# Performance work log

Hardware: AMD Instinct MI355X
Metric: run time of the kernel (lower is better)

Reference implementation:

```python
import jax, jax.numpy as jnp
import numpy as np

FMAP = 160        # feature-map side -> N = FMAP*FMAP anchors
STRIDE = 4.0      # anchor grid stride in pixels
ANCHOR_SIZE = 32.0
NUM_CLASSES = 8
MAX_GT = 50
BATCH = 32


def setup_inputs() -> dict:
    key = jax.random.key(0)
    k0, k1, k2, k3, k4, k5 = jax.random.split(key, 6)
    B, C, H = BATCH, NUM_CLASSES, FMAP
    cls_output = jax.random.normal(k0, (B, C, 1, H, H), jnp.float32)
    reg_output = jax.random.normal(k1, (B, 4, 1, H, H), jnp.float32) * 0.3
    # anchor grid: one ANCHOR_SIZE box per feature-map cell; flatten order
    # matches torch's reshape over (H, W)
    c = (jnp.arange(H, dtype=jnp.float32) + 0.5) * STRIDE
    cy, cx = jnp.meshgrid(c, c, indexing='ij')   # row-major [H, W]
    cx = cx.reshape(-1); cy = cy.reshape(-1)
    half = ANCHOR_SIZE / 2.0
    anchors = jnp.stack([cx - half, cy - half, cx + half, cy + half], axis=1)
    # padded GT boxes, all geometrically valid (x1<x2, y1<y2)
    cxy = jax.random.uniform(k2, (B, MAX_GT, 2), jnp.float32, 64.0, 576.0)
    wh = jax.random.uniform(k3, (B, MAX_GT, 2), jnp.float32, 16.0, 128.0)
    gt_boxes = jnp.concatenate([cxy - wh / 2.0, cxy + wh / 2.0], axis=-1)
    gt_labels = jax.random.randint(k4, (B, MAX_GT), 0, NUM_CLASSES)
    num_boxes = jax.random.randint(k5, (B,), 0, MAX_GT + 1)
    return dict(cls_output=cls_output, reg_output=reg_output, anchors=anchors,
                gt_boxes=gt_boxes, gt_labels=gt_labels, num_boxes=num_boxes)


def _decode_boxes(reg, anchors):
    # inverse of the encoding in the loss: tx=(gt_cx-a_cx)*(4/aw) then (tx+1)/2
    aw = anchors[:, 2] - anchors[:, 0]
    ah = anchors[:, 3] - anchors[:, 1]
    acx = anchors[:, 0] + 0.5 * aw
    acy = anchors[:, 1] + 0.5 * ah
    tx = reg[..., 0] * 2.0 - 1.0
    ty = reg[..., 1] * 2.0 - 1.0
    cx = acx + tx * aw / 4.0
    cy = acy + ty * ah / 4.0
    w = aw * jnp.exp(reg[..., 2])
    h = ah * jnp.exp(reg[..., 3])
    return jnp.stack([cx - w / 2, cy - h / 2, cx + w / 2, cy + h / 2], axis=-1)


def _pairwise_iou(b1, b2):
    # b1 [B,N,4], b2 [B,M,4] -> [B,N,M]
    lt = jnp.maximum(b1[:, :, None, :2], b2[:, None, :, :2])
    rb = jnp.minimum(b1[:, :, None, 2:], b2[:, None, :, 2:])
    wh = jnp.clip(rb - lt, 0.0)
    inter = wh[..., 0] * wh[..., 1]
    a1 = (b1[..., 2] - b1[..., 0]) * (b1[..., 3] - b1[..., 1])
    a2 = (b2[..., 2] - b2[..., 0]) * (b2[..., 3] - b2[..., 1])
    return inter / jnp.maximum(a1[:, :, None] + a2[:, None, :] - inter, 1e-8)


def _smooth_l1(x):
    ax = jnp.abs(x)
    return jnp.where(ax < 1.0, 0.5 * x * x, ax - 0.5)


def _forward(cls_output, reg_output, anchors, gt_boxes, gt_labels, num_boxes):
    B, C = cls_output.shape[0], cls_output.shape[1]
    M = gt_boxes.shape[1]
    cls_i = cls_output.reshape(B, C, -1).transpose(0, 2, 1)   # [B,N,C]
    reg_i = reg_output.reshape(B, 4, -1).transpose(0, 2, 1)   # [B,N,4]
    decoded = _decode_boxes(reg_i, anchors)                    # [B,N,4]
    ious = _pairwise_iou(decoded, gt_boxes)                    # [B,N,M]
    valid = jnp.arange(M)[None, :] < num_boxes[:, None]        # [B,M]
    ious = jnp.where(valid[:, None, :], ious, -1.0)
    max_ious = ious.max(axis=-1)                               # [B,N]
    max_idx = ious.argmax(axis=-1)                             # [B,N]
    has = num_boxes > 0                                        # [B]
    pos = (max_ious >= 0.25) & has[:, None]
    neg = (max_ious < 0.1) & has[:, None]
    # classification
    logp = jax.nn.log_softmax(cls_i, axis=-1)
    tgt = jnp.take_along_axis(gt_labels, max_idx, axis=1)      # [B,N]
    ce_tgt = -jnp.take_along_axis(logp, tgt[..., None], axis=-1)[..., 0]
    ce_bg = -logp[..., 0]
    posf = pos.astype(cls_i.dtype)
    negf = neg.astype(cls_i.dtype)
    npos = posf.sum(-1)
    nneg = negf.sum(-1)
    cls_pos = jnp.where(npos > 0, (ce_tgt * posf).sum(-1) / jnp.maximum(npos, 1.0), 0.0)
    cls_neg = jnp.where(nneg > 0, (ce_bg * negf).sum(-1) / jnp.maximum(nneg, 1.0), 0.0)
    cls_losses = jnp.where(has, cls_pos + cls_neg, ce_bg.mean(-1))
    pg = jnp.take_along_axis(gt_boxes, max_idx[..., None], axis=1)  # [B,N,4]
    aw = anchors[:, 2] - anchors[:, 0]
    ah = anchors[:, 3] - anchors[:, 1]
    acx = anchors[:, 0] + 0.5 * aw
    acy = anchors[:, 1] + 0.5 * ah
    gw = pg[..., 2] - pg[..., 0]
    gh = pg[..., 3] - pg[..., 1]
    gcx = pg[..., 0] + 0.5 * gw
    gcy = pg[..., 1] + 0.5 * gh
    tx = ((gcx - acx) * (4.0 / aw) + 1.0) / 2.0
    ty = ((gcy - acy) * (4.0 / ah) + 1.0) / 2.0
    tw = jnp.log(jnp.maximum(gw, 1e-6) / aw)
    th = jnp.log(jnp.maximum(gh, 1e-6) / ah)
    reg_t = jnp.stack([tx, ty, tw, th], axis=-1)               # [B,N,4]
    sl = _smooth_l1(reg_i - reg_t)
    reg_losses = jnp.where(npos > 0,
                           (sl * posf[..., None]).sum((-1, -2)) / jnp.maximum(npos * 4.0, 1.0),
                           0.0)
    total_pos = npos.sum()
    cls_final = cls_losses.mean()
    reg_final = reg_losses.sum() / jnp.maximum(total_pos, 1.0)
    return cls_final + reg_final, cls_final, reg_final, total_pos


def reference(cls_output, reg_output, anchors, gt_boxes, gt_labels, num_boxes):
    return _forward(cls_output, reg_output, anchors, gt_boxes, gt_labels, num_boxes)
```

## Files before the change

kernel.cpp:

```cpp
#include <hip/hip_runtime.h>

#define FMAP 160
#define NANCH (FMAP * FMAP)
#define NCLS 8
#define MAXGT 50
#define BATCH 32
#define NT 256
#define TILES 5
#define BLOCKS_PER_B (TILES * TILES)
#define PSTRIDE 8

__device__ __forceinline__ float fc(const float4& v, int k) {
    return k == 0 ? v.x : k == 1 ? v.y : k == 2 ? v.z : v.w;
}
__device__ __forceinline__ float sl1(float x) {
    float ax = fabsf(x);
    return ax < 1.f ? 0.5f * x * x : ax - 0.5f;
}

__global__ __launch_bounds__(NT) void detloss_main(
    const float* __restrict__ cls, const float* __restrict__ reg,
    const float* __restrict__ gtb, const int* __restrict__ gtl,
    const int* __restrict__ nb, float* __restrict__ partials)
{
    const int b  = blockIdx.y;
    const int t  = threadIdx.x;
    const int bx = blockIdx.x;
    const int tx = bx % TILES, ty = bx / TILES;
    const int w  = t >> 6, l = t & 63;
    const int R  = ty * 32 + w * 8 + (l >> 3);
    const int G  = tx * 8 + (l & 7);
    const int vt = R * (FMAP / 4) + G;

    const float4* regv = (const float4*)(reg + (size_t)b * 4 * NANCH);
    float4 rx = regv[0 * (NANCH / 4) + vt];
    float4 ry = regv[1 * (NANCH / 4) + vt];
    float4 rw = regv[2 * (NANCH / 4) + vt];
    float4 rh = regv[3 * (NANCH / 4) + vt];
    const float4* clsv = (const float4*)(cls + (size_t)b * NCLS * NANCH);
    float4 L[NCLS];
#pragma unroll
    for (int c = 0; c < NCLS; c++) L[c] = clsv[c * (NANCH / 4) + vt];

    __shared__ float4 gbox[64];
    __shared__ float  garea[64];
    __shared__ int    glab[64];
    if (t < MAXGT) {
        float4 g = ((const float4*)gtb)[b * MAXGT + t];
        gbox[t]  = g;
        garea[t] = (g.z - g.x) * (g.w - g.y);
        glab[t]  = gtl[b * MAXGT + t];
    }
    const int num = nb[b];

    const float acx0 = (float)((G * 4) * 4 + 2);
    const float acy  = (float)(R * 4 + 2);

    float x0[4], y0[4], x1[4], y1[4], a1[4];
#pragma unroll
    for (int k = 0; k < 4; k++) {
        float acx = acx0 + 4.f * (float)k;
        float txr = fc(rx, k) * 2.f - 1.f;
        float tyr = fc(ry, k) * 2.f - 1.f;
        float cx = acx + txr * 8.f;
        float cy = acy + tyr * 8.f;
        float ww = 32.f * __expf(fc(rw, k));
        float hh = 32.f * __expf(fc(rh, k));
        x0[k] = cx - 0.5f * ww; y0[k] = cy - 0.5f * hh;
        x1[k] = cx + 0.5f * ww; y1[k] = cy + 0.5f * hh;
        a1[k] = ww * hh;
    }

    float lse[4], cebg[4];
#pragma unroll
    for (int k = 0; k < 4; k++) {
        float s = 0.f;
#pragma unroll
        for (int c = 0; c < NCLS; c++) s += __expf(fc(L[c], k));
        lse[k]  = __logf(s);
        cebg[k] = lse[k] - fc(L[0], k);
    }

    float bx0 = fminf(fminf(x0[0], x0[1]), fminf(x0[2], x0[3]));
    float by0 = fminf(fminf(y0[0], y0[1]), fminf(y0[2], y0[3]));
    float bx1 = fmaxf(fmaxf(x1[0], x1[1]), fmaxf(x1[2], x1[3]));
    float by1 = fmaxf(fmaxf(y1[0], y1[1]), fmaxf(y1[2], y1[3]));
#pragma unroll
    for (int o = 1; o < 64; o <<= 1) {
        bx0 = fminf(bx0, __shfl_xor(bx0, o, 64));
        by0 = fminf(by0, __shfl_xor(by0, o, 64));
        bx1 = fmaxf(bx1, __shfl_xor(bx1, o, 64));
        by1 = fmaxf(by1, __shfl_xor(by1, o, 64));
    }

    __syncthreads();

    float4 gme = gbox[l];
    bool pass = (l < num) && (gme.x <= bx1) && (gme.z >= bx0)
                          && (gme.y <= by1) && (gme.w >= by0);
    unsigned long long mask = __ballot(pass);

    float bi[4] = {-1.f, -1.f, -1.f, -1.f};
    float bu[4] = { 1.f,  1.f,  1.f,  1.f};
    int   bidx[4] = {0, 0, 0, 0};
    while (mask) {
        int m = (int)__builtin_ctzll(mask);
        mask &= mask - 1;
        float4 g  = gbox[m];
        float  ga = garea[m];
#pragma unroll
        for (int k = 0; k < 4; k++) {
            float ltx = fmaxf(x0[k], g.x), lty = fmaxf(y0[k], g.y);
            float rbx = fminf(x1[k], g.z), rby = fminf(y1[k], g.w);
            float wx = fmaxf(rbx - ltx, 0.f), wy = fmaxf(rby - lty, 0.f);
            float inter = wx * wy;
            float u = a1[k] + ga - inter;
            bool better = inter * bu[k] > bi[k] * u;
            bi[k]   = better ? inter : bi[k];
            bu[k]   = better ? u     : bu[k];
            bidx[k] = better ? m     : bidx[k];
        }
    }

    float s_pk = 0.f, s_cp = 0.f, s_cn = 0.f, s_bg = 0.f, s_sl = 0.f;
    const bool has = num > 0;
#pragma unroll
    for (int k = 0; k < 4; k++) {
        s_bg += cebg[k];
        bool pos = has && (bi[k] >= 0.25f * bu[k]);
        bool neg = has && (bi[k] < 0.1f * bu[k]);
        s_pk += pos ? 1.f : (neg ? 4096.f : 0.f);
        s_cn += neg ? cebg[k] : 0.f;
        if (pos) {
            int tg = glab[bidx[k]];
            float e0 = (tg & 1) ? fc(L[1], k) : fc(L[0], k);
            float e1 = (tg & 1) ? fc(L[3], k) : fc(L[2], k);
            float e2 = (tg & 1) ? fc(L[5], k) : fc(L[4], k);
            float e3 = (tg & 1) ? fc(L[7], k) : fc(L[6], k);
            float f0 = (tg & 2) ? e1 : e0;
            float f1 = (tg & 2) ? e3 : e2;
            float ltg = (tg & 4) ? f1 : f0;
            s_cp += lse[k] - ltg;
            float4 gp = gbox[bidx[k]];
            float gw = gp.z - gp.x, gh = gp.w - gp.y;
            float gcx = gp.x + 0.5f * gw, gcy = gp.y + 0.5f * gh;
            float acx = acx0 + 4.f * (float)k;
            float txt = ((gcx - acx) * 0.125f + 1.f) * 0.5f;
            float tyt = ((gcy - acy) * 0.125f + 1.f) * 0.5f;
            float twt = __logf(fmaxf(gw, 1e-6f) * 0.03125f);
            float tht = __logf(fmaxf(gh, 1e-6f) * 0.03125f);
            s_sl += sl1(fc(rx, k) - txt) + sl1(fc(ry, k) - tyt)
                  + sl1(fc(rw, k) - twt) + sl1(fc(rh, k) - tht);
        }
    }

#pragma unroll
    for (int o = 32; o > 0; o >>= 1) {
        s_pk += __shfl_down(s_pk, o, 64);
        s_cp += __shfl_down(s_cp, o, 64);
        s_cn += __shfl_down(s_cn, o, 64);
        s_bg += __shfl_down(s_bg, o, 64);
        s_sl += __shfl_down(s_sl, o, 64);
    }
    __shared__ float red[4][5];
    if (l == 0) {
        red[w][0] = s_pk; red[w][1] = s_cp; red[w][2] = s_cn;
        red[w][3] = s_bg; red[w][4] = s_sl;
    }
    __syncthreads();
    if (t == 0) {
        float* p = partials + (size_t)(b * BLOCKS_PER_B + bx) * PSTRIDE;
        float4 v = make_float4(red[0][0] + red[1][0] + red[2][0] + red[3][0],
                               red[0][1] + red[1][1] + red[2][1] + red[3][1],
                               red[0][2] + red[1][2] + red[2][2] + red[3][2],
                               red[0][3] + red[1][3] + red[2][3] + red[3][3]);
        *(float4*)p = v;
        p[4] = red[0][4] + red[1][4] + red[2][4] + red[3][4];
    }
}

__global__ __launch_bounds__(256) void detloss_final(
    const float* __restrict__ partials, const int* __restrict__ nb,
    float* __restrict__ out)
{
    const int t = threadIdx.x;
    const int img = t >> 3, sub = t & 7;
    float np = 0.f, nn = 0.f, cp = 0.f, cn = 0.f, bg = 0.f, sl = 0.f;
#pragma unroll
    for (int j = 0; j < 4; ++j) {
        int blk = sub + (j << 3);
        if (blk < BLOCKS_PER_B) {
            const float* p = partials + (size_t)(img * BLOCKS_PER_B + blk) * PSTRIDE;
            float pk  = p[0];
            float nnv = floorf(pk * (1.f / 4096.f));
            np += pk - 4096.f * nnv;
            nn += nnv;
            cp += p[1]; cn += p[2]; bg += p[3]; sl += p[4];
        }
    }
#pragma unroll
    for (int o = 4; o > 0; o >>= 1) {
        np += __shfl_down(np, o, 8);
        nn += __shfl_down(nn, o, 8);
        cp += __shfl_down(cp, o, 8);
        cn += __shfl_down(cn, o, 8);
        bg += __shfl_down(bg, o, 8);
        sl += __shfl_down(sl, o, 8);
    }
    __shared__ float acc[32][4];
    if (sub == 0) {
        bool hasb = nb[img] > 0;
        float clsb;
        if (hasb) {
            float a = (np > 0.f) ? cp / fmaxf(np, 1.f) : 0.f;
            float c = (nn > 0.f) ? cn / fmaxf(nn, 1.f) : 0.f;
            clsb = a + c;
        } else {
            clsb = bg / (float)NANCH;
        }
        float regb = (np > 0.f) ? sl / fmaxf(np * 4.f, 1.f) : 0.f;
        acc[img][0] = clsb; acc[img][1] = regb; acc[img][2] = np;
    }
    __syncthreads();
    if (t < 64) {
        float c = 0.f, r = 0.f, tp = 0.f;
        if (t < 32) { c = acc[t][0]; r = acc[t][1]; tp = acc[t][2]; }
#pragma unroll
        for (int o = 32; o > 0; o >>= 1) {
            c  += __shfl_down(c,  o, 64);
            r  += __shfl_down(r,  o, 64);
            tp += __shfl_down(tp, o, 64);
        }
        if (t == 0) {
            float clsf = c / (float)BATCH;
            float regf = r / fmaxf(tp, 1.f);
            out[0] = clsf + regf;
            out[1] = clsf;
            out[2] = regf;
            out[3] = tp;
        }
    }
}

extern "C" void kernel_launch(void* const* d_in, const int* in_sizes, int n_in,
                              void* d_out, int out_size, void* d_ws, size_t ws_size,
                              hipStream_t stream) {
    const float* cls = (const float*)d_in[0];
    const float* reg = (const float*)d_in[1];
    const float* gtb = (const float*)d_in[3];
    const int*   gtl = (const int*)d_in[4];
    const int*   nb  = (const int*)d_in[5];
    float* out      = (float*)d_out;
    float* partials = (float*)d_ws;

    dim3 grid(BLOCKS_PER_B, BATCH);
    detloss_main<<<grid, NT, 0, stream>>>(cls, reg, gtb, gtl, nb, partials);
    detloss_final<<<1, 256, 0, stream>>>(partials, nb, out);
}
```

Before: 19.53 us.

## Fuse main and final kernels via cooperative launch with grid sync

Moves the per-tile work and the final reduction into device functions and runs them in one cooperative kernel separated by a grid-wide barrier, so the second kernel launch goes away. A fallback to the two-kernel path stays in place for when occupancy cannot hold all 800 blocks at once. Each call now adds host-side occupancy and attribute queries, and the cooperative launch plus grid sync carry their own overhead.

```diff
diff --git a/kernel.cpp b/kernel.cpp
--- a/kernel.cpp
+++ b/kernel.cpp
@@ -1,4 +1,7 @@
 #include <hip/hip_runtime.h>
+#include <hip/hip_cooperative_groups.h>
+
+namespace cg = cooperative_groups;
 
 #define FMAP 160
 #define NANCH (FMAP * FMAP)
@@ -18,14 +21,12 @@
     return ax < 1.f ? 0.5f * x * x : ax - 0.5f;
 }
 
-__global__ __launch_bounds__(NT) void detloss_main(
+__device__ __forceinline__ void tile_work(
     const float* __restrict__ cls, const float* __restrict__ reg,
     const float* __restrict__ gtb, const int* __restrict__ gtl,
-    const int* __restrict__ nb, float* __restrict__ partials)
-{
-    const int b  = blockIdx.y;
-    const int t  = threadIdx.x;
-    const int bx = blockIdx.x;
+    const int* __restrict__ nb, float* __restrict__ partials,
+    int b, int bx, int t)
+{
     const int tx = bx % TILES, ty = bx / TILES;
     const int w  = t >> 6, l = t & 63;
     const int R  = ty * 32 + w * 8 + (l >> 3);
@@ -176,14 +177,14 @@
                                red[0][3] + red[1][3] + red[2][3] + red[3][3]);
         *(float4*)p = v;
         p[4] = red[0][4] + red[1][4] + red[2][4] + red[3][4];
-    }
-}
-
-__global__ __launch_bounds__(256) void detloss_final(
+        __threadfence();
+    }
+}
+
+__device__ __forceinline__ void finalize_work(
     const float* __restrict__ partials, const int* __restrict__ nb,
-    float* __restrict__ out)
-{
-    const int t = threadIdx.x;
+    float* __restrict__ out, int t)
+{
     const int img = t >> 3, sub = t & 7;
     float np = 0.f, nn = 0.f, cp = 0.f, cn = 0.f, bg = 0.f, sl = 0.f;
 #pragma unroll
@@ -242,6 +243,33 @@
     }
 }
 
+__global__ __launch_bounds__(NT, 4) void detloss_coop(
+    const float* __restrict__ cls, const float* __restrict__ reg,
+    const float* __restrict__ gtb, const int* __restrict__ gtl,
+    const int* __restrict__ nb, float* __restrict__ partials,
+    float* __restrict__ out)
+{
+    tile_work(cls, reg, gtb, gtl, nb, partials, blockIdx.y, blockIdx.x, threadIdx.x);
+    cg::this_grid().sync();
+    if (blockIdx.x == 0 && blockIdx.y == 0)
+        finalize_work(partials, nb, out, threadIdx.x);
+}
+
+__global__ __launch_bounds__(NT) void detloss_main(
+    const float* __restrict__ cls, const float* __restrict__ reg,
+    const float* __restrict__ gtb, const int* __restrict__ gtl,
+    const int* __restrict__ nb, float* __restrict__ partials)
+{
+    tile_work(cls, reg, gtb, gtl, nb, partials, blockIdx.y, blockIdx.x, threadIdx.x);
+}
+
+__global__ __launch_bounds__(NT) void detloss_final(
+    const float* __restrict__ partials, const int* __restrict__ nb,
+    float* __restrict__ out)
+{
+    finalize_work(partials, nb, out, threadIdx.x);
+}
+
 extern "C" void kernel_launch(void* const* d_in, const int* in_sizes, int n_in,
                               void* d_out, int out_size, void* d_ws, size_t ws_size,
                               hipStream_t stream) {
@@ -254,6 +282,20 @@
     float* partials = (float*)d_ws;
 
     dim3 grid(BLOCKS_PER_B, BATCH);
-    detloss_main<<<grid, NT, 0, stream>>>(cls, reg, gtb, gtl, nb, partials);
-    detloss_final<<<1, 256, 0, stream>>>(partials, nb, out);
-}
+
+    int maxBlocksPerCU = 0, ncu = 0, dev = 0;
+    hipGetDevice(&dev);
+    hipDeviceGetAttribute(&ncu, hipDeviceAttributeMultiprocessorCount, dev);
+    hipError_t qe = hipOccupancyMaxActiveBlocksPerMultiprocessor(
+        &maxBlocksPerCU, (const void*)detloss_coop, NT, 0);
+
+    if (qe == hipSuccess && (long)maxBlocksPerCU * ncu >= BLOCKS_PER_B * BATCH) {
+        void* args[] = { (void*)&cls, (void*)&reg, (void*)&gtb, (void*)&gtl,
+                         (void*)&nb, (void*)&partials, (void*)&out };
+        hipLaunchCooperativeKernel((const void*)detloss_coop, grid, dim3(NT),
+                                   args, 0, stream);
+    } else {
+        detloss_main<<<grid, NT, 0, stream>>>(cls, reg, gtb, gtl, nb, partials);
+        detloss_final<<<1, NT, 0, stream>>>(partials, nb, out);
+    }
+}
```

Result: slower. 27.72 us (+41.9%).

## Halve anchors per thread with float2 loads and double block count

Applied to the files above, without the earlier changes.

Each thread now handles 2 anchors via float2 loads instead of 4 via float4, and the grid grows from 25 to 50 blocks per image with 16x16-anchor-column tiles. This doubles the thread count to raise occupancy and latency hiding, and shrinks per-wave bounding boxes so the GT culling ballot passes fewer boxes. In exchange it issues narrower loads, repeats the GT smem setup and block reductions twice as often, and has the final kernel read twice as many partials.

```diff
diff --git a/kernel.cpp b/kernel.cpp
--- a/kernel.cpp
+++ b/kernel.cpp
@@ -6,12 +6,13 @@
 #define MAXGT 50
 #define BATCH 32
 #define NT 256
-#define TILES 5
-#define BLOCKS_PER_B (TILES * TILES)
+#define TILES_X 5
+#define TILES_Y 10
+#define BLOCKS_PER_B (TILES_X * TILES_Y)
 #define PSTRIDE 8
 
-__device__ __forceinline__ float fc(const float4& v, int k) {
-    return k == 0 ? v.x : k == 1 ? v.y : k == 2 ? v.z : v.w;
+__device__ __forceinline__ float fc2(const float2& v, int k) {
+    return k == 0 ? v.x : v.y;
 }
 __device__ __forceinline__ float sl1(float x) {
     float ax = fabsf(x);
@@ -26,21 +27,21 @@
     const int b  = blockIdx.y;
     const int t  = threadIdx.x;
     const int bx = blockIdx.x;
-    const int tx = bx % TILES, ty = bx / TILES;
+    const int tx = bx % TILES_X, ty = bx / TILES_X;
     const int w  = t >> 6, l = t & 63;
-    const int R  = ty * 32 + w * 8 + (l >> 3);
-    const int G  = tx * 8 + (l & 7);
-    const int vt = R * (FMAP / 4) + G;
-
-    const float4* regv = (const float4*)(reg + (size_t)b * 4 * NANCH);
-    float4 rx = regv[0 * (NANCH / 4) + vt];
-    float4 ry = regv[1 * (NANCH / 4) + vt];
-    float4 rw = regv[2 * (NANCH / 4) + vt];
-    float4 rh = regv[3 * (NANCH / 4) + vt];
-    const float4* clsv = (const float4*)(cls + (size_t)b * NCLS * NANCH);
-    float4 L[NCLS];
-#pragma unroll
-    for (int c = 0; c < NCLS; c++) L[c] = clsv[c * (NANCH / 4) + vt];
+    const int R  = ty * 16 + w * 4 + (l >> 4);
+    const int C  = tx * 16 + (l & 15);
+    const int vt = R * (FMAP / 2) + C;
+
+    const float2* regv = (const float2*)(reg + (size_t)b * 4 * NANCH);
+    float2 rx = regv[0 * (NANCH / 2) + vt];
+    float2 ry = regv[1 * (NANCH / 2) + vt];
+    float2 rw = regv[2 * (NANCH / 2) + vt];
+    float2 rh = regv[3 * (NANCH / 2) + vt];
+    const float2* clsv = (const float2*)(cls + (size_t)b * NCLS * NANCH);
+    float2 L[NCLS];
+#pragma unroll
+    for (int c = 0; c < NCLS; c++) L[c] = clsv[c * (NANCH / 2) + vt];
 
     __shared__ float4 gbox[64];
     __shared__ float  garea[64];
@@ -53,38 +54,38 @@
     }
     const int num = nb[b];
 
-    const float acx0 = (float)((G * 4) * 4 + 2);
+    const float acx0 = (float)((C * 2) * 4 + 2);
     const float acy  = (float)(R * 4 + 2);
 
-    float x0[4], y0[4], x1[4], y1[4], a1[4];
-#pragma unroll
-    for (int k = 0; k < 4; k++) {
+    float x0[2], y0[2], x1[2], y1[2], a1[2];
+#pragma unroll
+    for (int k = 0; k < 2; k++) {
         float acx = acx0 + 4.f * (float)k;
-        float txr = fc(rx, k) * 2.f - 1.f;
-        float tyr = fc(ry, k) * 2.f - 1.f;
+        float txr = fc2(rx, k) * 2.f - 1.f;
+        float tyr = fc2(ry, k) * 2.f - 1.f;
         float cx = acx + txr * 8.f;
         float cy = acy + tyr * 8.f;
-        float ww = 32.f * __expf(fc(rw, k));
-        float hh = 32.f * __expf(fc(rh, k));
+        float ww = 32.f * __expf(fc2(rw, k));
+        float hh = 32.f * __expf(fc2(rh, k));
         x0[k] = cx - 0.5f * ww; y0[k] = cy - 0.5f * hh;
         x1[k] = cx + 0.5f * ww; y1[k] = cy + 0.5f * hh;
         a1[k] = ww * hh;
     }
 
-    float lse[4], cebg[4];
-#pragma unroll
-    for (int k = 0; k < 4; k++) {
+    float lse[2], cebg[2];
+#pragma unroll
+    for (int k = 0; k < 2; k++) {
         float s = 0.f;
 #pragma unroll
-        for (int c = 0; c < NCLS; c++) s += __expf(fc(L[c], k));
+        for (int c = 0; c < NCLS; c++) s += __expf(fc2(L[c], k));
         lse[k]  = __logf(s);
-        cebg[k] = lse[k] - fc(L[0], k);
-    }
-
-    float bx0 = fminf(fminf(x0[0], x0[1]), fminf(x0[2], x0[3]));
-    float by0 = fminf(fminf(y0[0], y0[1]), fminf(y0[2], y0[3]));
-    float bx1 = fmaxf(fmaxf(x1[0], x1[1]), fmaxf(x1[2], x1[3]));
-    float by1 = fmaxf(fmaxf(y1[0], y1[1]), fmaxf(y1[2], y1[3]));
+        cebg[k] = lse[k] - fc2(L[0], k);
+    }
+
+    float bx0 = fminf(x0[0], x0[1]);
+    float by0 = fminf(y0[0], y0[1]);
+    float bx1 = fmaxf(x1[0], x1[1]);
+    float by1 = fmaxf(y1[0], y1[1]);
 #pragma unroll
     for (int o = 1; o < 64; o <<= 1) {
         bx0 = fminf(bx0, __shfl_xor(bx0, o, 64));
@@ -100,16 +101,16 @@
                           && (gme.y <= by1) && (gme.w >= by0);
     unsigned long long mask = __ballot(pass);
 
-    float bi[4] = {-1.f, -1.f, -1.f, -1.f};
-    float bu[4] = { 1.f,  1.f,  1.f,  1.f};
-    int   bidx[4] = {0, 0, 0, 0};
+    float bi[2] = {-1.f, -1.f};
+    float bu[2] = { 1.f,  1.f};
+    int   bidx[2] = {0, 0};
     while (mask) {
         int m = (int)__builtin_ctzll(mask);
         mask &= mask - 1;
         float4 g  = gbox[m];
         float  ga = garea[m];
 #pragma unroll
-        for (int k = 0; k < 4; k++) {
+        for (int k = 0; k < 2; k++) {
             float ltx = fmaxf(x0[k], g.x), lty = fmaxf(y0[k], g.y);
             float rbx = fminf(x1[k], g.z), rby = fminf(y1[k], g.w);
             float wx = fmaxf(rbx - ltx, 0.f), wy = fmaxf(rby - lty, 0.f);
@@ -125,7 +126,7 @@
     float s_pk = 0.f, s_cp = 0.f, s_cn = 0.f, s_bg = 0.f, s_sl = 0.f;
     const bool has = num > 0;
 #pragma unroll
-    for (int k = 0; k < 4; k++) {
+    for (int k = 0; k < 2; k++) {
         s_bg += cebg[k];
         bool pos = has && (bi[k] >= 0.25f * bu[k]);
         bool neg = has && (bi[k] < 0.1f * bu[k]);
@@ -133,10 +134,10 @@
         s_cn += neg ? cebg[k] : 0.f;
         if (pos) {
             int tg = glab[bidx[k]];
-            float e0 = (tg & 1) ? fc(L[1], k) : fc(L[0], k);
-            float e1 = (tg & 1) ? fc(L[3], k) : fc(L[2], k);
-            float e2 = (tg & 1) ? fc(L[5], k) : fc(L[4], k);
-            float e3 = (tg & 1) ? fc(L[7], k) : fc(L[6], k);
+            float e0 = (tg & 1) ? fc2(L[1], k) : fc2(L[0], k);
+            float e1 = (tg & 1) ? fc2(L[3], k) : fc2(L[2], k);
+            float e2 = (tg & 1) ? fc2(L[5], k) : fc2(L[4], k);
+            float e3 = (tg & 1) ? fc2(L[7], k) : fc2(L[6], k);
             float f0 = (tg & 2) ? e1 : e0;
             float f1 = (tg & 2) ? e3 : e2;
             float ltg = (tg & 4) ? f1 : f0;
@@ -149,8 +150,8 @@
             float tyt = ((gcy - acy) * 0.125f + 1.f) * 0.5f;
             float twt = __logf(fmaxf(gw, 1e-6f) * 0.03125f);
             float tht = __logf(fmaxf(gh, 1e-6f) * 0.03125f);
-            s_sl += sl1(fc(rx, k) - txt) + sl1(fc(ry, k) - tyt)
-                  + sl1(fc(rw, k) - twt) + sl1(fc(rh, k) - tht);
+            s_sl += sl1(fc2(rx, k) - txt) + sl1(fc2(ry, k) - tyt)
+                  + sl1(fc2(rw, k) - twt) + sl1(fc2(rh, k) - tht);
         }
     }
 
@@ -179,7 +180,7 @@
     }
 }
 
-__global__ __launch_bounds__(256) void detloss_final(
+__global__ __launch_bounds__(NT) void detloss_final(
     const float* __restrict__ partials, const int* __restrict__ nb,
     float* __restrict__ out)
 {
@@ -187,7 +188,7 @@
     const int img = t >> 3, sub = t & 7;
     float np = 0.f, nn = 0.f, cp = 0.f, cn = 0.f, bg = 0.f, sl = 0.f;
 #pragma unroll
-    for (int j = 0; j < 4; ++j) {
+    for (int j = 0; j < 7; ++j) {
         int blk = sub + (j << 3);
         if (blk < BLOCKS_PER_B) {
             const float* p = partials + (size_t)(img * BLOCKS_PER_B + blk) * PSTRIDE;
@@ -255,5 +256,5 @@
 
     dim3 grid(BLOCKS_PER_B, BATCH);
     detloss_main<<<grid, NT, 0, stream>>>(cls, reg, gtb, gtl, nb, partials);
-    detloss_final<<<1, 256, 0, stream>>>(partials, nb, out);
-}
+    detloss_final<<<1, NT, 0, stream>>>(partials, nb, out);
+}
```

Result: faster. 18.45 us (-5.5%).
